# Kernel optimization log

Hardware: AMD Instinct MI355X
Metric: run time of the kernel (lower is better)

Reference implementation:

```python
import jax, jax.numpy as jnp
import numpy as np

N_USERS = 50000
N_DISHES = 10000
N_EDGES = 200000
D_IN = 1024
HID = 256
OUT = 128


def _dense_params(key, d_in, d_out):
    kw, kb = jax.random.split(key)
    W = jax.random.normal(kw, (d_in, d_out), jnp.float32) * (1.0 / np.sqrt(d_in))
    b = jnp.zeros((d_out,), jnp.float32)
    return W, b


def setup_inputs() -> dict:
    key = jax.random.key(0)
    ks = jax.random.split(key, 12)
    inp = {
        "user_feat": jax.random.normal(ks[0], (N_USERS, D_IN), jnp.float32),
        "dish_feat": jax.random.normal(ks[1], (N_DISHES, D_IN), jnp.float32),
        "edge_user": jax.random.randint(ks[2], (N_EDGES,), 0, N_USERS, jnp.int32),
        "edge_dish": jax.random.randint(ks[3], (N_EDGES,), 0, N_DISHES, jnp.int32),
    }
    inp["W_ui"], inp["b_ui"] = _dense_params(ks[4], D_IN, HID)   # user_initial_proj
    inp["W_di"], inp["b_di"] = _dense_params(ks[5], D_IN, HID)   # dish_initial_proj
    inp["W_um"], inp["b_um"] = _dense_params(ks[6], D_IN, HID)   # user_message_fn (sender=dish)
    inp["W_dm"], inp["b_dm"] = _dense_params(ks[7], D_IN, HID)   # dish_message_fn (sender=user)
    inp["W_uu"], inp["b_uu"] = _dense_params(ks[8], HID, HID)    # user_update_fn
    inp["W_du"], inp["b_du"] = _dense_params(ks[9], HID, HID)    # dish_update_fn
    inp["W_up"], inp["b_up"] = _dense_params(ks[10], HID, OUT)   # user_proj
    inp["W_dp"], inp["b_dp"] = _dense_params(ks[11], HID, OUT)   # dish_proj
    return inp


def reference(user_feat, dish_feat, edge_user, edge_dish,
              W_ui, b_ui, W_di, b_di, W_um, b_um, W_dm, b_dm,
              W_uu, b_uu, W_du, b_du, W_up, b_up, W_dp, b_dp):
    # initial projections
    user_init = jax.nn.relu(user_feat @ W_ui + b_ui)   # [U, H]
    dish_init = jax.nn.relu(dish_feat @ W_di + b_di)   # [D, H]

    # SimpleConv on 'interacts_reverse': sender=dish, receiver=user
    u_msg = jax.nn.relu(dish_feat[edge_dish] @ W_um + b_um)          # [E, H]
    user_agg = jax.ops.segment_sum(u_msg, edge_user, num_segments=N_USERS)
    user_upd = jax.nn.relu((user_agg + user_init) @ W_uu + b_uu)
    user_emb = user_upd @ W_up + b_up                                 # [U, OUT]

    # SimpleConv on 'interacts': sender=user, receiver=dish
    d_msg = jax.nn.relu(user_feat[edge_user] @ W_dm + b_dm)          # [E, H]
    dish_agg = jax.ops.segment_sum(d_msg, edge_dish, num_segments=N_DISHES)
    dish_upd = jax.nn.relu((dish_agg + dish_init) @ W_du + b_du)
    dish_emb = dish_upd @ W_dp + b_dp                                 # [D, OUT]

    return (user_emb, dish_emb)
```

## Files before the change

### kernel.cpp

```cpp
#include <hip/hip_runtime.h>
#include <hip/hip_bf16.h>

#define D_IN  1024
#define HID   256
#define OUT_D 128

using bf16x8  = __attribute__((ext_vector_type(8))) short;
using bf16x4  = __attribute__((ext_vector_type(4))) short;
using f32x4   = __attribute__((ext_vector_type(4))) float;
typedef unsigned int u32;

__device__ inline float bf2f(short s) {
    unsigned u = ((unsigned)(unsigned short)s) << 16;
    return __uint_as_float(u);
}
__device__ inline short f2bf(float f) {
    __hip_bfloat16 h = __float2bfloat16(f);
    return *reinterpret_cast<short*>(&h);
}

__device__ __forceinline__ void gld16(void* lds, const void* g) {
    __builtin_amdgcn_global_load_lds(
        (const __attribute__((address_space(1))) u32*)g,
        (__attribute__((address_space(3))) u32*)lds, 16, 0, 0);
}

__global__ void pack_all(
    const float* __restrict__ W_ui, const float* __restrict__ W_dm,
    const float* __restrict__ W_di, const float* __restrict__ W_um,
    const float* __restrict__ W_uu, const float* __restrict__ W_du,
    const float* __restrict__ W_up, const float* __restrict__ W_dp,
    const float* __restrict__ b_ui, const float* __restrict__ b_dm,
    const float* __restrict__ b_di, const float* __restrict__ b_um,
    short* __restrict__ Wut, short* __restrict__ Wdt,
    short* __restrict__ Wuut, short* __restrict__ Wdut,
    short* __restrict__ Wupt, short* __restrict__ Wdpt,
    float* __restrict__ bu, float* __restrict__ bd)
{
    const int z = blockIdx.z;
    const int tx = threadIdx.x, ty = threadIdx.y;
    if (z == 8) {
        if (blockIdx.x != 0 || blockIdx.y != 0) return;
        int t = ty * 32 + tx;
        bu[t] = b_ui[t]; bu[256 + t] = b_dm[t];
        bd[t] = b_di[t]; bd[256 + t] = b_um[t];
        return;
    }
    const float* in; short* out; int K, N, n_off = 0;
    switch (z) {
        case 0: in = W_ui; out = Wut;  K = 1024; N = 256; n_off = 0;   break;
        case 1: in = W_dm; out = Wut;  K = 1024; N = 256; n_off = 256; break;
        case 2: in = W_di; out = Wdt;  K = 1024; N = 256; n_off = 0;   break;
        case 3: in = W_um; out = Wdt;  K = 1024; N = 256; n_off = 256; break;
        case 4: in = W_uu; out = Wuut; K = 256;  N = 256; break;
        case 5: in = W_du; out = Wdut; K = 256;  N = 256; break;
        case 6: in = W_up; out = Wupt; K = 256;  N = 128; break;
        default:in = W_dp; out = Wdpt; K = 256;  N = 128; break;
    }
    const int n0 = blockIdx.x * 32, k0 = blockIdx.y * 32;
    if (n0 >= N || k0 >= K) return;
    __shared__ float t[32][33];
#pragma unroll
    for (int j = 0; j < 32; j += 8)
        t[ty + j][tx] = in[(size_t)(k0 + ty + j) * N + (n0 + tx)];
    __syncthreads();
#pragma unroll
    for (int j = 0; j < 32; j += 8)
        out[(size_t)(n_off + n0 + ty + j) * K + (k0 + tx)] = f2bf(t[tx][ty + j]);
}

template <bool RELU, bool AF32, bool CF32>
__global__ __launch_bounds__(256) void mfma_gemm_bf16(
    const void* __restrict__ A, int lda,
    const short* __restrict__ Wt,
    const float* __restrict__ bias,
    void* __restrict__ Cvoid, int M, int N, int K, int nN)
{
    constexpr int ABYTES = AF32 ? 32768 : 16384;
    __shared__ __align__(16) char smem[ABYTES + 16384];
    char* AsB = smem;
    char* BsB = smem + ABYTES;

    const int tid = threadIdx.x;

    const int nwg = gridDim.x;
    const int orig = blockIdx.x;
    const int qq = nwg >> 3, rr = nwg & 7;
    const int xcd = orig & 7, pos = orig >> 3;
    const int wg = (xcd < rr) ? (xcd * (qq + 1) + pos)
                              : (rr * (qq + 1) + (xcd - rr) * qq + pos);
    const int n0 = (wg % nN) * 128;
    const int m0 = (wg / nN) * 128;

    const int w = tid >> 6, l = tid & 63;
    const int wm = (w >> 1) * 64, wn = (w & 1) * 64;
    const int fr = l & 15, fg = l >> 4;

    f32x4 acc[4][4] = {};

    const char* Abase = (const char*)A;
    const char* Bbase = (const char*)Wt;
    const size_t lda_b = (size_t)lda * (AF32 ? 4 : 2);
    const size_t ldb_b = (size_t)K * 2;

    for (int k0 = 0; k0 < K; k0 += 64) {
        if (AF32) {
#pragma unroll
            for (int i = 0; i < 8; ++i) {
                int o = i * 4096 + tid * 16;
                int row = o >> 8, cb = o & 255;
                int scb = cb ^ ((row & 7) << 4);
                int arow = m0 + row; if (arow > M - 1) arow = M - 1;
                gld16(AsB + o, Abase + (size_t)arow * lda_b + (size_t)k0 * 4 + scb);
            }
        } else {
#pragma unroll
            for (int i = 0; i < 4; ++i) {
                int o = i * 4096 + tid * 16;
                int row = o >> 7, cb = o & 127;
                int scb = cb ^ ((row & 7) << 4);
                int arow = m0 + row; if (arow > M - 1) arow = M - 1;
                gld16(AsB + o, Abase + (size_t)arow * lda_b + (size_t)k0 * 2 + scb);
            }
        }
#pragma unroll
        for (int i = 0; i < 4; ++i) {
            int o = i * 4096 + tid * 16;
            int row = o >> 7, cb = o & 127;
            int scb = cb ^ ((row & 7) << 4);
            gld16(BsB + o, Bbase + (size_t)(n0 + row) * ldb_b + (size_t)k0 * 2 + scb);
        }
        __syncthreads();

#pragma unroll
        for (int kk = 0; kk < 2; ++kk) {
            bf16x8 af[4], bfv[4];
#pragma unroll
            for (int i = 0; i < 4; ++i) {
                int row = wm + i * 16 + fr;
                if (AF32) {
                    int cbase = kk * 128 + fg * 32;
                    int c1 = cbase ^ ((row & 7) << 4);
                    int c2 = (cbase + 16) ^ ((row & 7) << 4);
                    const char* rb = AsB + row * 256;
                    f32x4 lo = *reinterpret_cast<const f32x4*>(rb + c1);
                    f32x4 hi = *reinterpret_cast<const f32x4*>(rb + c2);
                    bf16x8 t;
                    t[0] = f2bf(lo[0]); t[1] = f2bf(lo[1]);
                    t[2] = f2bf(lo[2]); t[3] = f2bf(lo[3]);
                    t[4] = f2bf(hi[0]); t[5] = f2bf(hi[1]);
                    t[6] = f2bf(hi[2]); t[7] = f2bf(hi[3]);
                    af[i] = t;
                } else {
                    int cb = (kk * 64 + fg * 16) ^ ((row & 7) << 4);
                    af[i] = *reinterpret_cast<const bf16x8*>(AsB + row * 128 + cb);
                }
            }
#pragma unroll
            for (int j = 0; j < 4; ++j) {
                int row = wn + j * 16 + fr;
                int cb = (kk * 64 + fg * 16) ^ ((row & 7) << 4);
                bfv[j] = *reinterpret_cast<const bf16x8*>(BsB + row * 128 + cb);
            }
#pragma unroll
            for (int i = 0; i < 4; ++i)
#pragma unroll
                for (int j = 0; j < 4; ++j)
                    acc[i][j] = __builtin_amdgcn_mfma_f32_16x16x32_bf16(
                        af[i], bfv[j], acc[i][j], 0, 0, 0);
        }
        __syncthreads();
    }

#pragma unroll
    for (int i = 0; i < 4; ++i) {
#pragma unroll
        for (int e = 0; e < 4; ++e) {
            int gm = m0 + wm + i * 16 + fg * 4 + e;
            if (gm >= M) continue;
#pragma unroll
            for (int j = 0; j < 4; ++j) {
                int gn = n0 + wn + j * 16 + fr;
                float v = acc[i][j][e] + bias[gn];
                if (RELU) v = fmaxf(v, 0.f);
                if (CF32) ((float*)Cvoid)[(size_t)gm * N + gn] = v;
                else      ((short*)Cvoid)[(size_t)gm * N + gn] = f2bf(v);
            }
        }
    }
}

__global__ void hist2(const int* __restrict__ eu, const int* __restrict__ ed,
                      int* __restrict__ cu, int* __restrict__ cd, int E)
{
    int i = blockIdx.x * blockDim.x + threadIdx.x;
    if (i < E) atomicAdd(&cu[eu[i]], 1);
    else if (i < 2 * E) atomicAdd(&cd[ed[i - E]], 1);
}

__global__ __launch_bounds__(1024) void scan2(
    const int* __restrict__ cnt_u, int* __restrict__ offs_u, int U,
    const int* __restrict__ cnt_d, int* __restrict__ offs_d, int D)
{
    const int* cnt = (blockIdx.x == 0) ? cnt_u : cnt_d;
    int* offs      = (blockIdx.x == 0) ? offs_u : offs_d;
    const int n    = (blockIdx.x == 0) ? U : D;

    __shared__ int tsum[1024];
    const int t = threadIdx.x;
    const int chunk = (n + 1023) / 1024;
    const int lo = t * chunk;
    const int hi = min(lo + chunk, n);
    int s = 0;
    for (int i = lo; i < hi; ++i) s += cnt[i];
    tsum[t] = s;
    __syncthreads();
    for (int d = 1; d < 1024; d <<= 1) {
        int v = (t >= d) ? tsum[t - d] : 0;
        __syncthreads();
        tsum[t] += v;
        __syncthreads();
    }
    int run = (t > 0) ? tsum[t - 1] : 0;
    for (int i = lo; i < hi; ++i) {
        offs[i] = run;
        run += cnt[i];
    }
}

__global__ void fill2(const int* __restrict__ eu, const int* __restrict__ ed,
                      int* __restrict__ offs_u, int* __restrict__ srcl_u,
                      int* __restrict__ offs_d, int* __restrict__ srcl_d, int E)
{
    int i = blockIdx.x * blockDim.x + threadIdx.x;
    if (i < E) {
        int p = atomicAdd(&offs_u[eu[i]], 1);
        srcl_u[p] = ed[i];
    } else if (i < 2 * E) {
        int k = i - E;
        int p = atomicAdd(&offs_d[ed[k]], 1);
        srcl_d[p] = eu[k];
    }
}

__global__ __launch_bounds__(256) void seg_sum_both(
    const short* __restrict__ dish_msg, const short* __restrict__ user_msg,
    const int* __restrict__ srcl_u, const int* __restrict__ offs_u,
    const int* __restrict__ cnt_u,
    const int* __restrict__ srcl_d, const int* __restrict__ offs_d,
    const int* __restrict__ cnt_d,
    short* __restrict__ user_buf, short* __restrict__ dish_buf,
    int U, int D, int nbU)
{
    const short* msg; const int *sl, *oe, *ct; short* acc; int nRows, rb;
    if (blockIdx.x < nbU) {
        msg = dish_msg; sl = srcl_u; oe = offs_u; ct = cnt_u;
        acc = user_buf; nRows = U; rb = blockIdx.x;
    } else {
        msg = user_msg; sl = srcl_d; oe = offs_d; ct = cnt_d;
        acc = dish_buf; nRows = D; rb = blockIdx.x - nbU;
    }
    int row = rb * 4 + (threadIdx.x >> 6);
    if (row >= nRows) return;
    const int lane = threadIdx.x & 63;
    const int deg = ct[row];
    if (deg == 0) return;
    const int base = oe[row] - deg;

    float s0 = 0.f, s1 = 0.f, s2 = 0.f, s3 = 0.f;
    int j = 0;
    for (; j + 4 <= deg; j += 4) {
        int i0 = sl[base + j], i1 = sl[base + j + 1];
        int i2 = sl[base + j + 2], i3 = sl[base + j + 3];
        bf16x4 v0 = *(const bf16x4*)&msg[(size_t)i0 * 512 + lane * 4];
        bf16x4 v1 = *(const bf16x4*)&msg[(size_t)i1 * 512 + lane * 4];
        bf16x4 v2 = *(const bf16x4*)&msg[(size_t)i2 * 512 + lane * 4];
        bf16x4 v3 = *(const bf16x4*)&msg[(size_t)i3 * 512 + lane * 4];
        s0 += bf2f(v0[0]) + bf2f(v1[0]) + bf2f(v2[0]) + bf2f(v3[0]);
        s1 += bf2f(v0[1]) + bf2f(v1[1]) + bf2f(v2[1]) + bf2f(v3[1]);
        s2 += bf2f(v0[2]) + bf2f(v1[2]) + bf2f(v2[2]) + bf2f(v3[2]);
        s3 += bf2f(v0[3]) + bf2f(v1[3]) + bf2f(v2[3]) + bf2f(v3[3]);
    }
    for (; j < deg; ++j) {
        int i0 = sl[base + j];
        bf16x4 v = *(const bf16x4*)&msg[(size_t)i0 * 512 + lane * 4];
        s0 += bf2f(v[0]); s1 += bf2f(v[1]); s2 += bf2f(v[2]); s3 += bf2f(v[3]);
    }
    bf16x4 c = *(bf16x4*)&acc[(size_t)row * 512 + lane * 4];
    c[0] = f2bf(bf2f(c[0]) + s0);
    c[1] = f2bf(bf2f(c[1]) + s1);
    c[2] = f2bf(bf2f(c[2]) + s2);
    c[3] = f2bf(bf2f(c[3]) + s3);
    *(bf16x4*)&acc[(size_t)row * 512 + lane * 4] = c;
}

extern "C" void kernel_launch(void* const* d_in, const int* in_sizes, int n_in,
                              void* d_out, int out_size, void* d_ws, size_t ws_size,
                              hipStream_t stream)
{
    const float* user_feat = (const float*)d_in[0];
    const float* dish_feat = (const float*)d_in[1];
    const int*   edge_user = (const int*)d_in[2];
    const int*   edge_dish = (const int*)d_in[3];
    const float* W_ui = (const float*)d_in[4];  const float* b_ui = (const float*)d_in[5];
    const float* W_di = (const float*)d_in[6];  const float* b_di = (const float*)d_in[7];
    const float* W_um = (const float*)d_in[8];  const float* b_um = (const float*)d_in[9];
    const float* W_dm = (const float*)d_in[10]; const float* b_dm = (const float*)d_in[11];
    const float* W_uu = (const float*)d_in[12]; const float* b_uu = (const float*)d_in[13];
    const float* W_du = (const float*)d_in[14]; const float* b_du = (const float*)d_in[15];
    const float* W_up = (const float*)d_in[16]; const float* b_up = (const float*)d_in[17];
    const float* W_dp = (const float*)d_in[18]; const float* b_dp = (const float*)d_in[19];

    const int U = in_sizes[0] / D_IN;
    const int D = in_sizes[1] / D_IN;
    const int E = in_sizes[2];

    float* out = (float*)d_out;
    float* user_emb = out;
    float* dish_emb = out + (size_t)U * OUT_D;

    short* sws = (short*)d_ws;
    short* user_buf = sws;
    short* dish_buf = user_buf + (size_t)U * 512;
    short* user_upd = dish_buf + (size_t)D * 512;
    short* dish_upd = user_upd + (size_t)U * 256;
    short* Wut  = dish_upd + (size_t)D * 256;
    short* Wdt  = Wut  + (size_t)512 * 1024;
    short* Wuut = Wdt  + (size_t)512 * 1024;
    short* Wdut = Wuut + (size_t)256 * 256;
    short* Wupt = Wdut + (size_t)256 * 256;
    short* Wdpt = Wupt + (size_t)128 * 256;
    float* bu   = (float*)(Wdpt + (size_t)128 * 256);
    float* bd   = bu + 512;
    int*   cnt_u  = (int*)(bd + 512);
    int*   cnt_d  = cnt_u + U;
    int*   offs_u = cnt_d + D;
    int*   offs_d = offs_u + U;
    int*   srcl_u = offs_d + D;
    int*   srcl_d = srcl_u + E;

    hipLaunchKernelGGL(pack_all, dim3(8, 32, 9), dim3(32, 8), 0, stream,
                       W_ui, W_dm, W_di, W_um, W_uu, W_du, W_up, W_dp,
                       b_ui, b_dm, b_di, b_um,
                       Wut, Wdt, Wuut, Wdut, Wupt, Wdpt, bu, bd);

    hipMemsetAsync(cnt_u, 0, (size_t)(U + D) * sizeof(int), stream);
    int eg2 = (2 * E + 255) / 256;
    hipLaunchKernelGGL(hist2, dim3(eg2), dim3(256), 0, stream,
                       edge_user, edge_dish, cnt_u, cnt_d, E);
    hipLaunchKernelGGL(scan2, dim3(2), dim3(1024), 0, stream,
                       cnt_u, offs_u, U, cnt_d, offs_d, D);
    hipLaunchKernelGGL(fill2, dim3(eg2), dim3(256), 0, stream,
                       edge_user, edge_dish, offs_u, srcl_u, offs_d, srcl_d, E);

    hipLaunchKernelGGL((mfma_gemm_bf16<true, true, false>),
                       dim3(((U + 127) / 128) * 4), dim3(256), 0, stream,
                       user_feat, D_IN, Wut, bu, user_buf, U, 512, D_IN, 4);
    hipLaunchKernelGGL((mfma_gemm_bf16<true, true, false>),
                       dim3(((D + 127) / 128) * 4), dim3(256), 0, stream,
                       dish_feat, D_IN, Wdt, bd, dish_buf, D, 512, D_IN, 4);

    int nbU = (U + 3) / 4;
    hipLaunchKernelGGL(seg_sum_both, dim3(nbU + (D + 3) / 4), dim3(256), 0, stream,
                       dish_buf + HID, user_buf + HID,
                       srcl_u, offs_u, cnt_u, srcl_d, offs_d, cnt_d,
                       user_buf, dish_buf, U, D, nbU);

    hipLaunchKernelGGL((mfma_gemm_bf16<true, false, false>),
                       dim3(((U + 127) / 128) * 2), dim3(256), 0, stream,
                       user_buf, 512, Wuut, b_uu, user_upd, U, HID, HID, 2);
    hipLaunchKernelGGL((mfma_gemm_bf16<true, false, false>),
                       dim3(((D + 127) / 128) * 2), dim3(256), 0, stream,
                       dish_buf, 512, Wdut, b_du, dish_upd, D, HID, HID, 2);

    hipLaunchKernelGGL((mfma_gemm_bf16<false, false, true>),
                       dim3((U + 127) / 128), dim3(256), 0, stream,
                       user_upd, HID, Wupt, b_up, user_emb, U, OUT_D, HID, 1);
    hipLaunchKernelGGL((mfma_gemm_bf16<false, false, true>),
                       dim3((D + 127) / 128), dim3(256), 0, stream,
                       dish_upd, HID, Wdpt, b_dp, dish_emb, D, OUT_D, HID, 1);
}
```

Before: 372.3 us.

## Double-buffer LDS tiles in MFMA GEMM with BK=32 prefetch of next stage

Result: slower. 395.1 us (+6.1%).

```diff
diff --git a/kernel.cpp b/kernel.cpp
--- a/kernel.cpp
+++ b/kernel.cpp
@@ -76,10 +76,11 @@
     const float* __restrict__ bias,
     void* __restrict__ Cvoid, int M, int N, int K, int nN)
 {
-    constexpr int ABYTES = AF32 ? 32768 : 16384;
-    __shared__ __align__(16) char smem[ABYTES + 16384];
-    char* AsB = smem;
-    char* BsB = smem + ABYTES;
+    constexpr int BK = 32;
+    constexpr int ABYTES = AF32 ? (128 * BK * 4) : (128 * BK * 2);
+    constexpr int BBYTES = 128 * BK * 2;
+    constexpr int STEP = ABYTES + BBYTES;
+    __shared__ __align__(16) char smem[2 * STEP];
 
     const int tid = threadIdx.x;
 
@@ -103,73 +104,81 @@
     const size_t lda_b = (size_t)lda * (AF32 ? 4 : 2);
     const size_t ldb_b = (size_t)K * 2;
 
-    for (int k0 = 0; k0 < K; k0 += 64) {
-        if (AF32) {
-#pragma unroll
-            for (int i = 0; i < 8; ++i) {
-                int o = i * 4096 + tid * 16;
-                int row = o >> 8, cb = o & 255;
-                int scb = cb ^ ((row & 7) << 4);
-                int arow = m0 + row; if (arow > M - 1) arow = M - 1;
-                gld16(AsB + o, Abase + (size_t)arow * lda_b + (size_t)k0 * 4 + scb);
-            }
-        } else {
+    auto stage = [&](int buf, int k0) {
+        char* As = smem + buf * STEP;
+        char* Bs = As + ABYTES;
+        if constexpr (AF32) {
 #pragma unroll
             for (int i = 0; i < 4; ++i) {
                 int o = i * 4096 + tid * 16;
                 int row = o >> 7, cb = o & 127;
                 int scb = cb ^ ((row & 7) << 4);
                 int arow = m0 + row; if (arow > M - 1) arow = M - 1;
-                gld16(AsB + o, Abase + (size_t)arow * lda_b + (size_t)k0 * 2 + scb);
+                gld16(As + o, Abase + (size_t)arow * lda_b + (size_t)k0 * 4 + scb);
             }
-        }
+        } else {
+#pragma unroll
+            for (int i = 0; i < 2; ++i) {
+                int o = i * 4096 + tid * 16;
+                int row = o >> 6, cb = o & 63;
+                int scb = cb ^ ((row & 3) << 4);
+                int arow = m0 + row; if (arow > M - 1) arow = M - 1;
+                gld16(As + o, Abase + (size_t)arow * lda_b + (size_t)k0 * 2 + scb);
+            }
+        }
+#pragma unroll
+        for (int i = 0; i < 2; ++i) {
+            int o = i * 4096 + tid * 16;
+            int row = o >> 6, cb = o & 63;
+            int scb = cb ^ ((row & 3) << 4);
+            gld16(Bs + o, Bbase + (size_t)(n0 + row) * ldb_b + (size_t)k0 * 2 + scb);
+        }
+    };
+
+    stage(0, 0);
+    __syncthreads();
+
+    int cur = 0;
+    for (int k0 = 0; k0 < K; k0 += BK) {
+        if (k0 + BK < K) stage(cur ^ 1, k0 + BK);
+
+        const char* As = smem + cur * STEP;
+        const char* Bs = As + ABYTES;
+        bf16x8 af[4], bfv[4];
 #pragma unroll
         for (int i = 0; i < 4; ++i) {
-            int o = i * 4096 + tid * 16;
-            int row = o >> 7, cb = o & 127;
-            int scb = cb ^ ((row & 7) << 4);
-            gld16(BsB + o, Bbase + (size_t)(n0 + row) * ldb_b + (size_t)k0 * 2 + scb);
-        }
+            int row = wm + i * 16 + fr;
+            if constexpr (AF32) {
+                int sw = (row & 7) << 4;
+                const char* rb = As + row * 128;
+                f32x4 lo = *reinterpret_cast<const f32x4*>(rb + ((fg * 32) ^ sw));
+                f32x4 hi = *reinterpret_cast<const f32x4*>(rb + ((fg * 32 + 16) ^ sw));
+                bf16x8 t;
+                t[0] = f2bf(lo[0]); t[1] = f2bf(lo[1]);
+                t[2] = f2bf(lo[2]); t[3] = f2bf(lo[3]);
+                t[4] = f2bf(hi[0]); t[5] = f2bf(hi[1]);
+                t[6] = f2bf(hi[2]); t[7] = f2bf(hi[3]);
+                af[i] = t;
+            } else {
+                int cb = (fg * 16) ^ ((row & 3) << 4);
+                af[i] = *reinterpret_cast<const bf16x8*>(As + row * 64 + cb);
+            }
+        }
+#pragma unroll
+        for (int j = 0; j < 4; ++j) {
+            int row = wn + j * 16 + fr;
+            int cb = (fg * 16) ^ ((row & 3) << 4);
+            bfv[j] = *reinterpret_cast<const bf16x8*>(Bs + row * 64 + cb);
+        }
+#pragma unroll
+        for (int i = 0; i < 4; ++i)
+#pragma unroll
+            for (int j = 0; j < 4; ++j)
+                acc[i][j] = __builtin_amdgcn_mfma_f32_16x16x32_bf16(
+                    af[i], bfv[j], acc[i][j], 0, 0, 0);
+
         __syncthreads();
-
-#pragma unroll
-        for (int kk = 0; kk < 2; ++kk) {
-            bf16x8 af[4], bfv[4];
-#pragma unroll
-            for (int i = 0; i < 4; ++i) {
-                int row = wm + i * 16 + fr;
-                if (AF32) {
-                    int cbase = kk * 128 + fg * 32;
-                    int c1 = cbase ^ ((row & 7) << 4);
-                    int c2 = (cbase + 16) ^ ((row & 7) << 4);
-                    const char* rb = AsB + row * 256;
-                    f32x4 lo = *reinterpret_cast<const f32x4*>(rb + c1);
-                    f32x4 hi = *reinterpret_cast<const f32x4*>(rb + c2);
-                    bf16x8 t;
-                    t[0] = f2bf(lo[0]); t[1] = f2bf(lo[1]);
-                    t[2] = f2bf(lo[2]); t[3] = f2bf(lo[3]);
-                    t[4] = f2bf(hi[0]); t[5] = f2bf(hi[1]);
-                    t[6] = f2bf(hi[2]); t[7] = f2bf(hi[3]);
-                    af[i] = t;
-                } else {
-                    int cb = (kk * 64 + fg * 16) ^ ((row & 7) << 4);
-                    af[i] = *reinterpret_cast<const bf16x8*>(AsB + row * 128 + cb);
-                }
-            }
-#pragma unroll
-            for (int j = 0; j < 4; ++j) {
-                int row = wn + j * 16 + fr;
-                int cb = (kk * 64 + fg * 16) ^ ((row & 7) << 4);
-                bfv[j] = *reinterpret_cast<const bf16x8*>(BsB + row * 128 + cb);
-            }
-#pragma unroll
-            for (int i = 0; i < 4; ++i)
-#pragma unroll
-                for (int j = 0; j < 4; ++j)
-                    acc[i][j] = __builtin_amdgcn_mfma_f32_16x16x32_bf16(
-                        af[i], bfv[j], acc[i][j], 0, 0, 0);
-        }
-        __syncthreads();
+        cur ^= 1;
     }
 
 #pragma unroll
```

## Replace LDS-staged GEMM with direct global-to-register MFMA loads and double buffering

Applied to the files above, without the earlier changes.

After: 658.8 us. 77.0% more time.

```diff
diff --git a/kernel.cpp b/kernel.cpp
--- a/kernel.cpp
+++ b/kernel.cpp
@@ -17,12 +17,6 @@
 __device__ inline short f2bf(float f) {
     __hip_bfloat16 h = __float2bfloat16(f);
     return *reinterpret_cast<short*>(&h);
-}
-
-__device__ __forceinline__ void gld16(void* lds, const void* g) {
-    __builtin_amdgcn_global_load_lds(
-        (const __attribute__((address_space(1))) u32*)g,
-        (__attribute__((address_space(3))) u32*)lds, 16, 0, 0);
 }
 
 __global__ void pack_all(
@@ -70,17 +64,12 @@
 }
 
 template <bool RELU, bool AF32, bool CF32>
-__global__ __launch_bounds__(256) void mfma_gemm_bf16(
-    const void* __restrict__ A, int lda,
+__global__ __launch_bounds__(256, AF32 ? 2 : 3) void mfma_gemm_direct(
+    const void* __restrict__ A_, int lda,
     const short* __restrict__ Wt,
     const float* __restrict__ bias,
     void* __restrict__ Cvoid, int M, int N, int K, int nN)
 {
-    constexpr int ABYTES = AF32 ? 32768 : 16384;
-    __shared__ __align__(16) char smem[ABYTES + 16384];
-    char* AsB = smem;
-    char* BsB = smem + ABYTES;
-
     const int tid = threadIdx.x;
 
     const int nwg = gridDim.x;
@@ -98,79 +87,91 @@
 
     f32x4 acc[4][4] = {};
 
-    const char* Abase = (const char*)A;
-    const char* Bbase = (const char*)Wt;
+    const char* Ab = (const char*)A_;
+    const char* Bb = (const char*)Wt;
     const size_t lda_b = (size_t)lda * (AF32 ? 4 : 2);
     const size_t ldb_b = (size_t)K * 2;
 
-    for (int k0 = 0; k0 < K; k0 += 64) {
-        if (AF32) {
-#pragma unroll
-            for (int i = 0; i < 8; ++i) {
-                int o = i * 4096 + tid * 16;
-                int row = o >> 8, cb = o & 255;
-                int scb = cb ^ ((row & 7) << 4);
-                int arow = m0 + row; if (arow > M - 1) arow = M - 1;
-                gld16(AsB + o, Abase + (size_t)arow * lda_b + (size_t)k0 * 4 + scb);
+    size_t aoff[4];
+    size_t boff[4];
+#pragma unroll
+    for (int i = 0; i < 4; ++i) {
+        int r = m0 + wm + i * 16 + fr;
+        if (r > M - 1) r = M - 1;
+        aoff[i] = (size_t)r * lda_b + (size_t)fg * (AF32 ? 32 : 16);
+    }
+#pragma unroll
+    for (int j = 0; j < 4; ++j) {
+        int r = n0 + wn + j * 16 + fr;
+        boff[j] = (size_t)r * ldb_b + (size_t)fg * 16;
+    }
+
+    const int T = K / 32;
+
+#define LOADB(BR, k0_) \
+    _Pragma("unroll") for (int j_ = 0; j_ < 4; ++j_) \
+        BR[j_] = *(const bf16x8*)(Bb + boff[j_] + (size_t)(k0_) * 2);
+
+#define LOADA32(AR, k0_) \
+    _Pragma("unroll") for (int i_ = 0; i_ < 4; ++i_) { \
+        AR[i_][0] = *(const f32x4*)(Ab + aoff[i_] + (size_t)(k0_) * 4); \
+        AR[i_][1] = *(const f32x4*)(Ab + aoff[i_] + (size_t)(k0_) * 4 + 16); }
+
+#define LOADA16(AR, k0_) \
+    _Pragma("unroll") for (int i_ = 0; i_ < 4; ++i_) \
+        AR[i_] = *(const bf16x8*)(Ab + aoff[i_] + (size_t)(k0_) * 2);
+
+#define COMPUTE32(AR, BR) \
+    _Pragma("unroll") for (int i_ = 0; i_ < 4; ++i_) { \
+        bf16x8 af_; \
+        af_[0] = f2bf(AR[i_][0][0]); af_[1] = f2bf(AR[i_][0][1]); \
+        af_[2] = f2bf(AR[i_][0][2]); af_[3] = f2bf(AR[i_][0][3]); \
+        af_[4] = f2bf(AR[i_][1][0]); af_[5] = f2bf(AR[i_][1][1]); \
+        af_[6] = f2bf(AR[i_][1][2]); af_[7] = f2bf(AR[i_][1][3]); \
+        _Pragma("unroll") for (int j_ = 0; j_ < 4; ++j_) \
+            acc[i_][j_] = __builtin_amdgcn_mfma_f32_16x16x32_bf16( \
+                af_, BR[j_], acc[i_][j_], 0, 0, 0); }
+
+#define COMPUTE16(AR, BR) \
+    _Pragma("unroll") for (int i_ = 0; i_ < 4; ++i_) \
+        _Pragma("unroll") for (int j_ = 0; j_ < 4; ++j_) \
+            acc[i_][j_] = __builtin_amdgcn_mfma_f32_16x16x32_bf16( \
+                AR[i_], BR[j_], acc[i_][j_], 0, 0, 0);
+
+    if constexpr (AF32) {
+        f32x4 aA[4][2], aB[4][2];
+        bf16x8 bA[4], bB[4];
+        LOADA32(aA, 0) LOADB(bA, 0)
+        for (int t = 0; t < T; t += 2) {
+            const int k1 = (t + 1) * 32;
+            LOADA32(aB, k1) LOADB(bB, k1)
+            COMPUTE32(aA, bA)
+            if (t + 2 < T) {
+                const int k2 = (t + 2) * 32;
+                LOADA32(aA, k2) LOADB(bA, k2)
             }
-        } else {
-#pragma unroll
-            for (int i = 0; i < 4; ++i) {
-                int o = i * 4096 + tid * 16;
-                int row = o >> 7, cb = o & 127;
-                int scb = cb ^ ((row & 7) << 4);
-                int arow = m0 + row; if (arow > M - 1) arow = M - 1;
-                gld16(AsB + o, Abase + (size_t)arow * lda_b + (size_t)k0 * 2 + scb);
+            COMPUTE32(aB, bB)
+        }
+    } else {
+        bf16x8 aA[4], aB[4];
+        bf16x8 bA[4], bB[4];
+        LOADA16(aA, 0) LOADB(bA, 0)
+        for (int t = 0; t < T; t += 2) {
+            const int k1 = (t + 1) * 32;
+            LOADA16(aB, k1) LOADB(bB, k1)
+            COMPUTE16(aA, bA)
+            if (t + 2 < T) {
+                const int k2 = (t + 2) * 32;
+                LOADA16(aA, k2) LOADB(bA, k2)
             }
+            COMPUTE16(aB, bB)
         }
-#pragma unroll
-        for (int i = 0; i < 4; ++i) {
-            int o = i * 4096 + tid * 16;
-            int row = o >> 7, cb = o & 127;
-            int scb = cb ^ ((row & 7) << 4);
-            gld16(BsB + o, Bbase + (size_t)(n0 + row) * ldb_b + (size_t)k0 * 2 + scb);
-        }
-        __syncthreads();
-
-#pragma unroll
-        for (int kk = 0; kk < 2; ++kk) {
-            bf16x8 af[4], bfv[4];
-#pragma unroll
-            for (int i = 0; i < 4; ++i) {
-                int row = wm + i * 16 + fr;
-                if (AF32) {
-                    int cbase = kk * 128 + fg * 32;
-                    int c1 = cbase ^ ((row & 7) << 4);
-                    int c2 = (cbase + 16) ^ ((row & 7) << 4);
-                    const char* rb = AsB + row * 256;
-                    f32x4 lo = *reinterpret_cast<const f32x4*>(rb + c1);
-                    f32x4 hi = *reinterpret_cast<const f32x4*>(rb + c2);
-                    bf16x8 t;
-                    t[0] = f2bf(lo[0]); t[1] = f2bf(lo[1]);
-                    t[2] = f2bf(lo[2]); t[3] = f2bf(lo[3]);
-                    t[4] = f2bf(hi[0]); t[5] = f2bf(hi[1]);
-                    t[6] = f2bf(hi[2]); t[7] = f2bf(hi[3]);
-                    af[i] = t;
-                } else {
-                    int cb = (kk * 64 + fg * 16) ^ ((row & 7) << 4);
-                    af[i] = *reinterpret_cast<const bf16x8*>(AsB + row * 128 + cb);
-                }
-            }
-#pragma unroll
-            for (int j = 0; j < 4; ++j) {
-                int row = wn + j * 16 + fr;
-                int cb = (kk * 64 + fg * 16) ^ ((row & 7) << 4);
-                bfv[j] = *reinterpret_cast<const bf16x8*>(BsB + row * 128 + cb);
-            }
-#pragma unroll
-            for (int i = 0; i < 4; ++i)
-#pragma unroll
-                for (int j = 0; j < 4; ++j)
-                    acc[i][j] = __builtin_amdgcn_mfma_f32_16x16x32_bf16(
-                        af[i], bfv[j], acc[i][j], 0, 0, 0);
-        }
-        __syncthreads();
-    }
+    }
+#undef LOADB
+#undef LOADA32
+#undef LOADA16
+#undef COMPUTE32
+#undef COMPUTE16
 
 #pragma unroll
     for (int i = 0; i < 4; ++i) {
@@ -353,10 +354,10 @@
     hipLaunchKernelGGL(fill2, dim3(eg2), dim3(256), 0, stream,
                        edge_user, edge_dish, offs_u, srcl_u, offs_d, srcl_d, E);
 
-    hipLaunchKernelGGL((mfma_gemm_bf16<true, true, false>),
+    hipLaunchKernelGGL((mfma_gemm_direct<true, true, false>),
                        dim3(((U + 127) / 128) * 4), dim3(256), 0, stream,
                        user_feat, D_IN, Wut, bu, user_buf, U, 512, D_IN, 4);
-    hipLaunchKernelGGL((mfma_gemm_bf16<true, true, false>),
+    hipLaunchKernelGGL((mfma_gemm_direct<true, true, false>),
                        dim3(((D + 127) / 128) * 4), dim3(256), 0, stream,
                        dish_feat, D_IN, Wdt, bd, dish_buf, D, 512, D_IN, 4);
 
@@ -366,17 +367,17 @@
                        srcl_u, offs_u, cnt_u, srcl_d, offs_d, cnt_d,
                        user_buf, dish_buf, U, D, nbU);
 
-    hipLaunchKernelGGL((mfma_gemm_bf16<true, false, false>),
+    hipLaunchKernelGGL((mfma_gemm_direct<true, false, false>),
                        dim3(((U + 127) / 128) * 2), dim3(256), 0, stream,
                        user_buf, 512, Wuut, b_uu, user_upd, U, HID, HID, 2);
-    hipLaunchKernelGGL((mfma_gemm_bf16<true, false, false>),
+    hipLaunchKernelGGL((mfma_gemm_direct<true, false, false>),
                        dim3(((D + 127) / 128) * 2), dim3(256), 0, stream,
                        dish_buf, 512, Wdut, b_du, dish_upd, D, HID, HID, 2);
 
-    hipLaunchKernelGGL((mfma_gemm_bf16<false, false, true>),
+    hipLaunchKernelGGL((mfma_gemm_direct<false, false, true>),
                        dim3((U + 127) / 128), dim3(256), 0, stream,
                        user_upd, HID, Wupt, b_up, user_emb, U, OUT_D, HID, 1);
-    hipLaunchKernelGGL((mfma_gemm_bf16<false, false, true>),
+    hipLaunchKernelGGL((mfma_gemm_direct<false, false, true>),
                        dim3((D + 127) / 128), dim3(256), 0, stream,
                        dish_upd, HID, Wdpt, b_dp, dish_emb, D, OUT_D, HID, 1);
 }
```

## Pipeline GEMM K-loop with register-staged A and double-buffered B tiles

Applied to the files above, without the earlier changes.

New measurement: 468.1 us. +25.8%, slower.

```diff
diff --git a/kernel.cpp b/kernel.cpp
--- a/kernel.cpp
+++ b/kernel.cpp
@@ -70,16 +70,14 @@
 }
 
 template <bool RELU, bool AF32, bool CF32>
-__global__ __launch_bounds__(256) void mfma_gemm_bf16(
-    const void* __restrict__ A, int lda,
+__global__ __launch_bounds__(256) void mfma_gemm_rs(
+    const void* __restrict__ A_, int lda,
     const short* __restrict__ Wt,
     const float* __restrict__ bias,
     void* __restrict__ Cvoid, int M, int N, int K, int nN)
 {
-    constexpr int ABYTES = AF32 ? 32768 : 16384;
-    __shared__ __align__(16) char smem[ABYTES + 16384];
-    char* AsB = smem;
-    char* BsB = smem + ABYTES;
+    __shared__ __align__(16) char As[16384];
+    __shared__ __align__(16) char Bs[2][16384];
 
     const int tid = threadIdx.x;
 
@@ -98,69 +96,81 @@
 
     f32x4 acc[4][4] = {};
 
-    const char* Abase = (const char*)A;
-    const char* Bbase = (const char*)Wt;
+    const char* Ab = (const char*)A_;
+    const char* Bb = (const char*)Wt;
     const size_t lda_b = (size_t)lda * (AF32 ? 4 : 2);
     const size_t ldb_b = (size_t)K * 2;
 
-    for (int k0 = 0; k0 < K; k0 += 64) {
-        if (AF32) {
-#pragma unroll
-            for (int i = 0; i < 8; ++i) {
-                int o = i * 4096 + tid * 16;
-                int row = o >> 8, cb = o & 255;
-                int scb = cb ^ ((row & 7) << 4);
-                int arow = m0 + row; if (arow > M - 1) arow = M - 1;
-                gld16(AsB + o, Abase + (size_t)arow * lda_b + (size_t)k0 * 4 + scb);
+    const int r_st = tid >> 1, h_st = tid & 1;
+    int arow = m0 + r_st; if (arow > M - 1) arow = M - 1;
+    const char* aSrcRow = Ab + (size_t)arow * lda_b;
+
+    f32x4  gA32[8];
+    bf16x8 gA16[4];
+
+    auto issueA = [&](int k0) {
+        if constexpr (AF32) {
+            const char* p = aSrcRow + (size_t)k0 * 4 + h_st * 128;
+#pragma unroll
+            for (int q = 0; q < 8; ++q) gA32[q] = *(const f32x4*)(p + q * 16);
+        } else {
+            const char* p = aSrcRow + (size_t)k0 * 2 + h_st * 64;
+#pragma unroll
+            for (int q = 0; q < 4; ++q) gA16[q] = *(const bf16x8*)(p + q * 16);
+        }
+    };
+    auto writeA = [&]() {
+#pragma unroll
+        for (int q = 0; q < 4; ++q) {
+            int slot = h_st * 4 + q;
+            int byte = r_st * 128 + ((slot * 16) ^ ((r_st & 7) << 4));
+            bf16x8 v;
+            if constexpr (AF32) {
+                f32x4 lo = gA32[2 * q], hi = gA32[2 * q + 1];
+                v[0] = f2bf(lo[0]); v[1] = f2bf(lo[1]);
+                v[2] = f2bf(lo[2]); v[3] = f2bf(lo[3]);
+                v[4] = f2bf(hi[0]); v[5] = f2bf(hi[1]);
+                v[6] = f2bf(hi[2]); v[7] = f2bf(hi[3]);
+            } else {
+                v = gA16[q];
             }
-        } else {
-#pragma unroll
-            for (int i = 0; i < 4; ++i) {
-                int o = i * 4096 + tid * 16;
-                int row = o >> 7, cb = o & 127;
-                int scb = cb ^ ((row & 7) << 4);
-                int arow = m0 + row; if (arow > M - 1) arow = M - 1;
-                gld16(AsB + o, Abase + (size_t)arow * lda_b + (size_t)k0 * 2 + scb);
-            }
-        }
+            *(bf16x8*)(As + byte) = v;
+        }
+    };
+    auto stageB = [&](int buf, int k0) {
 #pragma unroll
         for (int i = 0; i < 4; ++i) {
             int o = i * 4096 + tid * 16;
             int row = o >> 7, cb = o & 127;
             int scb = cb ^ ((row & 7) << 4);
-            gld16(BsB + o, Bbase + (size_t)(n0 + row) * ldb_b + (size_t)k0 * 2 + scb);
-        }
-        __syncthreads();
-
+            gld16(Bs[buf] + o, Bb + (size_t)(n0 + row) * ldb_b + (size_t)k0 * 2 + scb);
+        }
+    };
+
+    const int T = K / 64;
+
+    issueA(0); stageB(0, 0);
+    writeA();
+    __syncthreads();
+    if (T > 1) { issueA(64); stageB(1, 64); }
+
+    int cur = 0;
+    for (int t = 0; t < T; ++t) {
+        const char* Bc = Bs[cur];
 #pragma unroll
         for (int kk = 0; kk < 2; ++kk) {
             bf16x8 af[4], bfv[4];
 #pragma unroll
             for (int i = 0; i < 4; ++i) {
                 int row = wm + i * 16 + fr;
-                if (AF32) {
-                    int cbase = kk * 128 + fg * 32;
-                    int c1 = cbase ^ ((row & 7) << 4);
-                    int c2 = (cbase + 16) ^ ((row & 7) << 4);
-                    const char* rb = AsB + row * 256;
-                    f32x4 lo = *reinterpret_cast<const f32x4*>(rb + c1);
-                    f32x4 hi = *reinterpret_cast<const f32x4*>(rb + c2);
-                    bf16x8 t;
-                    t[0] = f2bf(lo[0]); t[1] = f2bf(lo[1]);
-                    t[2] = f2bf(lo[2]); t[3] = f2bf(lo[3]);
-                    t[4] = f2bf(hi[0]); t[5] = f2bf(hi[1]);
-                    t[6] = f2bf(hi[2]); t[7] = f2bf(hi[3]);
-                    af[i] = t;
-                } else {
-                    int cb = (kk * 64 + fg * 16) ^ ((row & 7) << 4);
-                    af[i] = *reinterpret_cast<const bf16x8*>(AsB + row * 128 + cb);
-                }
+                int cb = row * 128 + (((kk * 4 + fg) * 16) ^ ((row & 7) << 4));
+                af[i] = *reinterpret_cast<const bf16x8*>(As + cb);
             }
 #pragma unroll
             for (int j = 0; j < 4; ++j) {
                 int row = wn + j * 16 + fr;
-                int cb = (kk * 64 + fg * 16) ^ ((row & 7) << 4);
-                bfv[j] = *reinterpret_cast<const bf16x8*>(BsB + row * 128 + cb);
+                int cb = row * 128 + (((kk * 4 + fg) * 16) ^ ((row & 7) << 4));
+                bfv[j] = *reinterpret_cast<const bf16x8*>(Bc + cb);
             }
 #pragma unroll
             for (int i = 0; i < 4; ++i)
@@ -169,7 +179,14 @@
                     acc[i][j] = __builtin_amdgcn_mfma_f32_16x16x32_bf16(
                         af[i], bfv[j], acc[i][j], 0, 0, 0);
         }
-        __syncthreads();
+
+        if (t + 1 < T) {
+            __syncthreads();
+            writeA();
+            __syncthreads();
+            if (t + 2 < T) { issueA((t + 2) * 64); stageB(cur, (t + 2) * 64); }
+            cur ^= 1;
+        }
     }
 
 #pragma unroll
@@ -353,10 +370,10 @@
     hipLaunchKernelGGL(fill2, dim3(eg2), dim3(256), 0, stream,
                        edge_user, edge_dish, offs_u, srcl_u, offs_d, srcl_d, E);
 
-    hipLaunchKernelGGL((mfma_gemm_bf16<true, true, false>),
+    hipLaunchKernelGGL((mfma_gemm_rs<true, true, false>),
                        dim3(((U + 127) / 128) * 4), dim3(256), 0, stream,
                        user_feat, D_IN, Wut, bu, user_buf, U, 512, D_IN, 4);
-    hipLaunchKernelGGL((mfma_gemm_bf16<true, true, false>),
+    hipLaunchKernelGGL((mfma_gemm_rs<true, true, false>),
                        dim3(((D + 127) / 128) * 4), dim3(256), 0, stream,
                        dish_feat, D_IN, Wdt, bd, dish_buf, D, 512, D_IN, 4);
 
@@ -366,17 +383,17 @@
                        srcl_u, offs_u, cnt_u, srcl_d, offs_d, cnt_d,
                        user_buf, dish_buf, U, D, nbU);
 
-    hipLaunchKernelGGL((mfma_gemm_bf16<true, false, false>),
+    hipLaunchKernelGGL((mfma_gemm_rs<true, false, false>),
                        dim3(((U + 127) / 128) * 2), dim3(256), 0, stream,
                        user_buf, 512, Wuut, b_uu, user_upd, U, HID, HID, 2);
-    hipLaunchKernelGGL((mfma_gemm_bf16<true, false, false>),
+    hipLaunchKernelGGL((mfma_gemm_rs<true, false, false>),
                        dim3(((D + 127) / 128) * 2), dim3(256), 0, stream,
                        dish_buf, 512, Wdut, b_du, dish_upd, D, HID, HID, 2);
 
-    hipLaunchKernelGGL((mfma_gemm_bf16<false, false, true>),
+    hipLaunchKernelGGL((mfma_gemm_rs<false, false, true>),
                        dim3((U + 127) / 128), dim3(256), 0, stream,
                        user_upd, HID, Wupt, b_up, user_emb, U, OUT_D, HID, 1);
-    hipLaunchKernelGGL((mfma_gemm_bf16<false, false, true>),
+    hipLaunchKernelGGL((mfma_gemm_rs<false, false, true>),
                        dim3((D + 127) / 128), dim3(256), 0, stream,
                        dish_upd, HID, Wdpt, b_dp, dish_emb, D, OUT_D, HID, 1);
 }
```
